# Kernel optimization log

Measured on AMD Instinct MI355X. Metric: run time of the kernel, lower is better.

## Reference

```python
import jax, jax.numpy as jnp
import numpy as np

B, T, C, H = 4096, 4, 1024, 8
DH = C // H
SCALE = DH ** -0.5
LN_EPS = 1e-5


def setup_inputs() -> dict:
    key = jax.random.key(0)
    k1, k2, k3 = jax.random.split(key, 3)
    feats = jax.random.normal(k1, (B, T, C), dtype=jnp.float32)
    Wqkv = jax.random.normal(k2, (T, C, 3 * C), dtype=jnp.float32) * 0.02
    bqkv = jnp.zeros((T, 3 * C), dtype=jnp.float32)
    Wproj = jax.random.normal(k3, (T, C, C), dtype=jnp.float32) * 0.02
    bproj = jnp.zeros((T, C), dtype=jnp.float32)
    gamma = jnp.ones((C,), dtype=jnp.float32)
    beta = jnp.zeros((C,), dtype=jnp.float32)
    return {"feats": feats, "Wqkv": Wqkv, "bqkv": bqkv,
            "Wproj": Wproj, "bproj": bproj, "gamma": gamma, "beta": beta}


def reference(feats, Wqkv, bqkv, Wproj, bproj, gamma, beta):
    # Grouped per-task QKV projection: [B,T,C] x [T,C,3C] -> [B,T,3C]
    qkv = jnp.einsum('btc,tcd->btd', feats, Wqkv) + bqkv
    q, k, v = jnp.split(qkv, 3, axis=-1)           # each [B,T,C]
    q = q.reshape(B, T, H, DH)
    k = k.reshape(B, T, H, DH)
    v = v.reshape(B, T, H, DH)
    # Cross-task attention: scores[b, query_task, key_task, head]
    scores = jnp.einsum('bqhd,bkhd->bqkh', q, k) * SCALE
    attn = jax.nn.softmax(scores, axis=2)          # softmax over key-task dim
    ctx = jnp.einsum('bqkh,bkhd->bqhd', attn, v)   # [B,T,H,DH]
    ctx = ctx.reshape(B, T, C)
    # Grouped per-task output projection (dropout is identity in eval)
    ctx = jnp.einsum('btc,tcd->btd', ctx, Wproj) + bproj
    # Residual + shared LayerNorm over channel dim
    x = ctx + feats
    mu = jnp.mean(x, axis=-1, keepdims=True)
    var = jnp.mean(jnp.square(x - mu), axis=-1, keepdims=True)
    return (x - mu) * jax.lax.rsqrt(var + LN_EPS) * gamma + beta
```

## Files before the change

kernel.cpp:

```cpp
#include <hip/hip_runtime.h>
#include <hip/hip_bf16.h>
#include <cstdint>
#include <cstddef>

#define B_SZ 4096
#define T_SZ 4
#define C_SZ 1024
#define H_SZ 8
#define DH_SZ 128
#define NQKV 3072
#define SCALE_F 0.08838834764831845f

typedef float f32x4 __attribute__((ext_vector_type(4)));
typedef short s16x8 __attribute__((ext_vector_type(8)));

static __device__ __forceinline__ float bf2f(unsigned short u) {
    union { unsigned int i; float f; } x; x.i = ((unsigned int)u) << 16; return x.f;
}
static __device__ __forceinline__ unsigned short f2bf(float f) {
    union { unsigned int i; float f; } x; x.f = f;
    unsigned int r = x.i + 0x7FFFu + ((x.i >> 16) & 1u);
    return (unsigned short)(r >> 16);
}

typedef const __attribute__((address_space(1))) void* gas_ptr;
typedef __attribute__((address_space(3))) void* las_ptr;
static __device__ __forceinline__ void async16(const void* g, void* l) {
    __builtin_amdgcn_global_load_lds((gas_ptr)g, (las_ptr)l, 16, 0, 0);
}

__global__ __launch_bounds__(256) void cvt_f32_bf16(const float* __restrict__ src,
                                                    unsigned short* __restrict__ dst, int n4) {
    int i = blockIdx.x * 256 + threadIdx.x;
    if (i >= n4) return;
    float4 v = reinterpret_cast<const float4*>(src)[i];
    ushort4 o;
    o.x = f2bf(v.x); o.y = f2bf(v.y); o.z = f2bf(v.z); o.w = f2bf(v.w);
    reinterpret_cast<ushort4*>(dst)[i] = o;
}

__global__ __launch_bounds__(256) void transpose_cvt(const float* __restrict__ src,
                                                     unsigned short* __restrict__ dst,
                                                     int K, int N) {
    __shared__ float tile[32][33];
    const float* s = src + (size_t)blockIdx.z * K * N;
    unsigned short* d = dst + (size_t)blockIdx.z * K * N;
    int n0 = blockIdx.x * 32, k0 = blockIdx.y * 32;
    int tx = threadIdx.x, ty = threadIdx.y;
#pragma unroll
    for (int i = 0; i < 4; i++) {
        int k = k0 + ty + i * 8;
        tile[ty + i * 8][tx] = s[(size_t)k * N + n0 + tx];
    }
    __syncthreads();
#pragma unroll
    for (int i = 0; i < 4; i++) {
        int n = n0 + ty + i * 8;
        d[(size_t)n * K + k0 + tx] = f2bf(tile[tx][ty + i * 8]);
    }
}

template<int NSIZE, int EPI>
__global__ __launch_bounds__(256) void gemm_bf16(
    const unsigned short* __restrict__ A,
    const unsigned short* __restrict__ Bt,
    const float* __restrict__ bias,
    const float* __restrict__ resid,
    unsigned short* __restrict__ out_bf,
    float* __restrict__ out_f)
{
    constexpr int BM = 128, BN = 128, BK = 32;
    __shared__ unsigned short lA[BM * BK];
    __shared__ unsigned short lB[BN * BK];

    const int t   = blockIdx.z;
    const int m0  = blockIdx.y * BM;
    const int n0  = blockIdx.x * BN;
    const int tid = threadIdx.x;
    const int lane = tid & 63;
    const int wave = tid >> 6;
    const int wm = (wave >> 1) * 64;
    const int wn = (wave & 1) * 64;
    const int quad = lane >> 4;
    const int l16  = lane & 15;

    const unsigned short* Abase = A + (size_t)t * C_SZ;
    const unsigned short* Bbase = Bt + (size_t)t * NSIZE * C_SZ;

    const int j0 = wave * 2;
    const unsigned short* gA[2];
    const unsigned short* gB[2];
    unsigned short* lAdst[2];
    unsigned short* lBdst[2];
#pragma unroll
    for (int j = 0; j < 2; j++) {
        int slot = (j0 + j) * 64 + lane;
        int row = slot >> 2;
        int ch  = (slot & 3) ^ (row & 3);
        gA[j] = Abase + (size_t)(m0 + row) * (T_SZ * C_SZ) + ch * 8;
        gB[j] = Bbase + (size_t)(n0 + row) * C_SZ + ch * 8;
        lAdst[j] = &lA[(j0 + j) * 512];
        lBdst[j] = &lB[(j0 + j) * 512];
    }

    const int sw = quad ^ (l16 & 3);
    const s16x8* aP[4];
    const s16x8* bP[4];
#pragma unroll
    for (int i = 0; i < 4; i++) {
        aP[i] = reinterpret_cast<const s16x8*>(&lA[(wm + i * 16 + l16) * BK + sw * 8]);
        bP[i] = reinterpret_cast<const s16x8*>(&lB[(wn + i * 16 + l16) * BK + sw * 8]);
    }

    f32x4 acc[4][4] = {};

    for (int kk = 0; kk < C_SZ; kk += BK) {
        async16(gA[0] + kk, lAdst[0]);
        async16(gA[1] + kk, lAdst[1]);
        async16(gB[0] + kk, lBdst[0]);
        async16(gB[1] + kk, lBdst[1]);
        __syncthreads();

        s16x8 af[4], bfr[4];
#pragma unroll
        for (int i = 0; i < 4; i++) { af[i] = *aP[i]; bfr[i] = *bP[i]; }
#pragma unroll
        for (int mi = 0; mi < 4; mi++)
#pragma unroll
            for (int ni = 0; ni < 4; ni++)
                acc[mi][ni] = __builtin_amdgcn_mfma_f32_16x16x32_bf16(
                    af[mi], bfr[ni], acc[mi][ni], 0, 0, 0);
        __syncthreads();
    }

#pragma unroll
    for (int ni = 0; ni < 4; ni++) {
        int gn = n0 + wn + ni * 16 + l16;
        float bi = bias[t * NSIZE + gn];
#pragma unroll
        for (int mi = 0; mi < 4; mi++) {
#pragma unroll
            for (int r = 0; r < 4; r++) {
                int gm = m0 + wm + mi * 16 + quad * 4 + r;
                size_t o = (size_t)(gm * T_SZ + t) * NSIZE + gn;
                float v = acc[mi][ni][r] + bi;
                if (EPI == 0) {
                    out_bf[o] = f2bf(v);
                } else {
                    out_f[o] = v + resid[o];
                }
            }
        }
    }
}

__global__ __launch_bounds__(256) void attn_kernel(const unsigned short* __restrict__ qkv,
                                                   unsigned short* __restrict__ ctx) {
    int wave = threadIdx.x >> 6, lane = threadIdx.x & 63;
    int g = blockIdx.x * 4 + wave;
    int b = g >> 3, h = g & 7;
    int d0 = lane * 2;

    const unsigned short* base = qkv + (size_t)b * T_SZ * NQKV + h * DH_SZ + d0;
    float qf[4][2], kf[4][2], vf[4][2];
#pragma unroll
    for (int i = 0; i < 4; i++) {
        const unsigned short* p = base + (size_t)i * NQKV;
        qf[i][0] = bf2f(p[0]);          qf[i][1] = bf2f(p[1]);
        kf[i][0] = bf2f(p[C_SZ]);       kf[i][1] = bf2f(p[C_SZ + 1]);
        vf[i][0] = bf2f(p[2 * C_SZ]);   vf[i][1] = bf2f(p[2 * C_SZ + 1]);
    }
    float s[4][4];
#pragma unroll
    for (int i = 0; i < 4; i++)
#pragma unroll
        for (int j = 0; j < 4; j++) {
            float p = qf[i][0] * kf[j][0] + qf[i][1] * kf[j][1];
#pragma unroll
            for (int off = 32; off > 0; off >>= 1) p += __shfl_xor(p, off);
            s[i][j] = p * SCALE_F;
        }
#pragma unroll
    for (int i = 0; i < 4; i++) {
        float m = fmaxf(fmaxf(s[i][0], s[i][1]), fmaxf(s[i][2], s[i][3]));
        float e0 = __expf(s[i][0] - m), e1 = __expf(s[i][1] - m);
        float e2 = __expf(s[i][2] - m), e3 = __expf(s[i][3] - m);
        float inv = 1.0f / (e0 + e1 + e2 + e3);
        s[i][0] = e0 * inv; s[i][1] = e1 * inv; s[i][2] = e2 * inv; s[i][3] = e3 * inv;
    }
#pragma unroll
    for (int i = 0; i < 4; i++) {
        float o0 = s[i][0] * vf[0][0] + s[i][1] * vf[1][0] + s[i][2] * vf[2][0] + s[i][3] * vf[3][0];
        float o1 = s[i][0] * vf[0][1] + s[i][1] * vf[1][1] + s[i][2] * vf[2][1] + s[i][3] * vf[3][1];
        size_t o = (size_t)(b * T_SZ + i) * C_SZ + h * DH_SZ + d0;
        ctx[o] = f2bf(o0); ctx[o + 1] = f2bf(o1);
    }
}

__global__ __launch_bounds__(256) void ln_kernel(const float* __restrict__ y,
                                                 const float* __restrict__ gamma,
                                                 const float* __restrict__ beta,
                                                 float* __restrict__ out) {
    int row = blockIdx.x;
    int lane = threadIdx.x & 63, wave = threadIdx.x >> 6;
    float4 v = reinterpret_cast<const float4*>(y + (size_t)row * C_SZ)[threadIdx.x];
    float s  = v.x + v.y + v.z + v.w;
    float ss = v.x * v.x + v.y * v.y + v.z * v.z + v.w * v.w;
#pragma unroll
    for (int off = 32; off > 0; off >>= 1) { s += __shfl_xor(s, off); ss += __shfl_xor(ss, off); }
    __shared__ float red[8];
    if (lane == 0) { red[wave] = s; red[wave + 4] = ss; }
    __syncthreads();
    float S  = red[0] + red[1] + red[2] + red[3];
    float SS = red[4] + red[5] + red[6] + red[7];
    float mean = S * (1.0f / C_SZ);
    float var  = SS * (1.0f / C_SZ) - mean * mean;
    float inv  = rsqrtf(var + 1e-5f);
    float4 g  = reinterpret_cast<const float4*>(gamma)[threadIdx.x];
    float4 be = reinterpret_cast<const float4*>(beta)[threadIdx.x];
    float4 o;
    o.x = (v.x - mean) * inv * g.x + be.x;
    o.y = (v.y - mean) * inv * g.y + be.y;
    o.z = (v.z - mean) * inv * g.z + be.z;
    o.w = (v.w - mean) * inv * g.w + be.w;
    reinterpret_cast<float4*>(out + (size_t)row * C_SZ)[threadIdx.x] = o;
}

extern "C" void kernel_launch(void* const* d_in, const int* in_sizes, int n_in,
                              void* d_out, int out_size, void* d_ws, size_t ws_size,
                              hipStream_t stream) {
    const float* feats = (const float*)d_in[0];
    const float* Wqkv  = (const float*)d_in[1];
    const float* bqkv  = (const float*)d_in[2];
    const float* Wproj = (const float*)d_in[3];
    const float* bproj = (const float*)d_in[4];
    const float* gamma = (const float*)d_in[5];
    const float* beta  = (const float*)d_in[6];
    float* out = (float*)d_out;

    char* ws = (char*)d_ws;
    unsigned short* feats_bf = (unsigned short*)(ws);
    unsigned short* wqkv_t   = (unsigned short*)(ws + 33554432);
    unsigned short* wproj_t  = (unsigned short*)(ws + 58720256);
    unsigned short* qkv      = (unsigned short*)(ws + 67108864);
    unsigned short* ctx      = (unsigned short*)(ws + 167772160);
    float* ybuf              = (float*)(ws + 67108864);

    cvt_f32_bf16<<<16384, 256, 0, stream>>>(feats, feats_bf, (B_SZ * T_SZ * C_SZ) / 4);
    transpose_cvt<<<dim3(96, 32, 4), dim3(32, 8), 0, stream>>>(Wqkv, wqkv_t, C_SZ, NQKV);
    transpose_cvt<<<dim3(32, 32, 4), dim3(32, 8), 0, stream>>>(Wproj, wproj_t, C_SZ, C_SZ);

    gemm_bf16<NQKV, 0><<<dim3(NQKV / 128, B_SZ / 128, T_SZ), 256, 0, stream>>>(
        feats_bf, wqkv_t, bqkv, nullptr, qkv, nullptr);

    attn_kernel<<<(B_SZ * H_SZ) / 4, 256, 0, stream>>>(qkv, ctx);

    gemm_bf16<C_SZ, 1><<<dim3(C_SZ / 128, B_SZ / 128, T_SZ), 256, 0, stream>>>(
        ctx, wproj_t, bproj, feats, nullptr, ybuf);

    ln_kernel<<<B_SZ * T_SZ, 256, 0, stream>>>(ybuf, gamma, beta, out);
}
```

Before: 444.0 us.

## Double GEMM K-tile, vectorize epilogue via LDS transpose, widen attention loads

The GEMM K tile grows from 32 to 64 with an 8-way XOR swizzle, which halves the number of barrier-separated load/compute iterations. The epilogue now transposes each accumulator fragment through LDS so every lane writes four contiguous outputs (ushort4 or float4) and reads bias and residual as float4, replacing scattered scalar stores. The attention kernel loads and stores bf16 pairs as 32-bit words instead of separate 16-bit accesses. In exchange, LDS use doubles, each thread has more in-flight async loads, and the epilogue adds LDS round trips.

Result: no change. 444.2 us (+0.0%).

```diff
diff --git a/kernel.cpp b/kernel.cpp
--- a/kernel.cpp
+++ b/kernel.cpp
@@ -69,7 +69,7 @@
     unsigned short* __restrict__ out_bf,
     float* __restrict__ out_f)
 {
-    constexpr int BM = 128, BN = 128, BK = 32;
+    constexpr int BM = 128, BN = 128, BK = 64;
     __shared__ unsigned short lA[BM * BK];
     __shared__ unsigned short lB[BN * BK];
 
@@ -87,68 +87,78 @@
     const unsigned short* Abase = A + (size_t)t * C_SZ;
     const unsigned short* Bbase = Bt + (size_t)t * NSIZE * C_SZ;
 
-    const int j0 = wave * 2;
-    const unsigned short* gA[2];
-    const unsigned short* gB[2];
-    unsigned short* lAdst[2];
-    unsigned short* lBdst[2];
-#pragma unroll
-    for (int j = 0; j < 2; j++) {
+    const int j0 = wave * 4;
+    const unsigned short* gA[4];
+    const unsigned short* gB[4];
+    unsigned short* lAdst[4];
+    unsigned short* lBdst[4];
+#pragma unroll
+    for (int j = 0; j < 4; j++) {
         int slot = (j0 + j) * 64 + lane;
-        int row = slot >> 2;
-        int ch  = (slot & 3) ^ (row & 3);
+        int row  = slot >> 3;
+        int ch   = (slot & 7) ^ (row & 7);
         gA[j] = Abase + (size_t)(m0 + row) * (T_SZ * C_SZ) + ch * 8;
         gB[j] = Bbase + (size_t)(n0 + row) * C_SZ + ch * 8;
         lAdst[j] = &lA[(j0 + j) * 512];
         lBdst[j] = &lB[(j0 + j) * 512];
     }
 
-    const int sw = quad ^ (l16 & 3);
-    const s16x8* aP[4];
-    const s16x8* bP[4];
-#pragma unroll
-    for (int i = 0; i < 4; i++) {
-        aP[i] = reinterpret_cast<const s16x8*>(&lA[(wm + i * 16 + l16) * BK + sw * 8]);
-        bP[i] = reinterpret_cast<const s16x8*>(&lB[(wn + i * 16 + l16) * BK + sw * 8]);
-    }
+    const int swz0 = ((quad)     ^ (l16 & 7)) * 8;
+    const int swz1 = ((quad + 4) ^ (l16 & 7)) * 8;
 
     f32x4 acc[4][4] = {};
 
     for (int kk = 0; kk < C_SZ; kk += BK) {
-        async16(gA[0] + kk, lAdst[0]);
-        async16(gA[1] + kk, lAdst[1]);
-        async16(gB[0] + kk, lBdst[0]);
-        async16(gB[1] + kk, lBdst[1]);
+#pragma unroll
+        for (int j = 0; j < 4; j++) async16(gA[j] + kk, lAdst[j]);
+#pragma unroll
+        for (int j = 0; j < 4; j++) async16(gB[j] + kk, lBdst[j]);
         __syncthreads();
 
-        s16x8 af[4], bfr[4];
-#pragma unroll
-        for (int i = 0; i < 4; i++) { af[i] = *aP[i]; bfr[i] = *bP[i]; }
-#pragma unroll
-        for (int mi = 0; mi < 4; mi++)
-#pragma unroll
-            for (int ni = 0; ni < 4; ni++)
-                acc[mi][ni] = __builtin_amdgcn_mfma_f32_16x16x32_bf16(
-                    af[mi], bfr[ni], acc[mi][ni], 0, 0, 0);
+#pragma unroll
+        for (int ks = 0; ks < 2; ks++) {
+            const int sw = ks ? swz1 : swz0;
+            s16x8 af[4], bfr[4];
+#pragma unroll
+            for (int i = 0; i < 4; i++) {
+                af[i]  = *reinterpret_cast<const s16x8*>(&lA[(wm + i * 16 + l16) * BK + sw]);
+                bfr[i] = *reinterpret_cast<const s16x8*>(&lB[(wn + i * 16 + l16) * BK + sw]);
+            }
+#pragma unroll
+            for (int mi = 0; mi < 4; mi++)
+#pragma unroll
+                for (int ni = 0; ni < 4; ni++)
+                    acc[mi][ni] = __builtin_amdgcn_mfma_f32_16x16x32_bf16(
+                        af[mi], bfr[ni], acc[mi][ni], 0, 0, 0);
+        }
         __syncthreads();
     }
 
+    float* tb = reinterpret_cast<float*>(lA) + wave * 640;
 #pragma unroll
     for (int ni = 0; ni < 4; ni++) {
-        int gn = n0 + wn + ni * 16 + l16;
-        float bi = bias[t * NSIZE + gn];
+        int gn = n0 + wn + ni * 16 + quad * 4;
+        float4 bi4 = *reinterpret_cast<const float4*>(&bias[t * NSIZE + gn]);
 #pragma unroll
         for (int mi = 0; mi < 4; mi++) {
-#pragma unroll
-            for (int r = 0; r < 4; r++) {
-                int gm = m0 + wm + mi * 16 + quad * 4 + r;
-                size_t o = (size_t)(gm * T_SZ + t) * NSIZE + gn;
-                float v = acc[mi][ni][r] + bi;
-                if (EPI == 0) {
-                    out_bf[o] = f2bf(v);
-                } else {
-                    out_f[o] = v + resid[o];
-                }
+            float* buf = tb + (mi & 1) * 320;
+#pragma unroll
+            for (int r = 0; r < 4; r++)
+                buf[(quad * 4 + r) * 20 + l16] = acc[mi][ni][r];
+            f32x4 v = *reinterpret_cast<const f32x4*>(&buf[l16 * 20 + quad * 4]);
+            int gm = m0 + wm + mi * 16 + l16;
+            size_t o = (size_t)(gm * T_SZ + t) * NSIZE + gn;
+            if (EPI == 0) {
+                ushort4 pk;
+                pk.x = f2bf(v[0] + bi4.x); pk.y = f2bf(v[1] + bi4.y);
+                pk.z = f2bf(v[2] + bi4.z); pk.w = f2bf(v[3] + bi4.w);
+                *reinterpret_cast<ushort4*>(&out_bf[o]) = pk;
+            } else {
+                float4 r4 = *reinterpret_cast<const float4*>(&resid[o]);
+                float4 ov;
+                ov.x = v[0] + bi4.x + r4.x; ov.y = v[1] + bi4.y + r4.y;
+                ov.z = v[2] + bi4.z + r4.z; ov.w = v[3] + bi4.w + r4.w;
+                *reinterpret_cast<float4*>(&out_f[o]) = ov;
             }
         }
     }
@@ -166,9 +176,12 @@
 #pragma unroll
     for (int i = 0; i < 4; i++) {
         const unsigned short* p = base + (size_t)i * NQKV;
-        qf[i][0] = bf2f(p[0]);          qf[i][1] = bf2f(p[1]);
-        kf[i][0] = bf2f(p[C_SZ]);       kf[i][1] = bf2f(p[C_SZ + 1]);
-        vf[i][0] = bf2f(p[2 * C_SZ]);   vf[i][1] = bf2f(p[2 * C_SZ + 1]);
+        unsigned int uq = *reinterpret_cast<const unsigned int*>(p);
+        unsigned int uk = *reinterpret_cast<const unsigned int*>(p + C_SZ);
+        unsigned int uv = *reinterpret_cast<const unsigned int*>(p + 2 * C_SZ);
+        qf[i][0] = bf2f(uq & 0xffff); qf[i][1] = bf2f(uq >> 16);
+        kf[i][0] = bf2f(uk & 0xffff); kf[i][1] = bf2f(uk >> 16);
+        vf[i][0] = bf2f(uv & 0xffff); vf[i][1] = bf2f(uv >> 16);
     }
     float s[4][4];
 #pragma unroll
@@ -193,7 +206,8 @@
         float o0 = s[i][0] * vf[0][0] + s[i][1] * vf[1][0] + s[i][2] * vf[2][0] + s[i][3] * vf[3][0];
         float o1 = s[i][0] * vf[0][1] + s[i][1] * vf[1][1] + s[i][2] * vf[2][1] + s[i][3] * vf[3][1];
         size_t o = (size_t)(b * T_SZ + i) * C_SZ + h * DH_SZ + d0;
-        ctx[o] = f2bf(o0); ctx[o + 1] = f2bf(o1);
+        *reinterpret_cast<unsigned int*>(&ctx[o]) =
+            (unsigned int)f2bf(o0) | ((unsigned int)f2bf(o1) << 16);
     }
 }
 
```
